# Performance work log

Hardware: AMD Instinct MI355X
Metric: run time of the kernel (lower is better)

Reference implementation:

```python
import jax, jax.numpy as jnp
import numpy as np

IN_CH, OUT_CH, K, N = 32, 64, 7, 64  # input_channels, output_channels, kernel_size, input_size


def _pad_kernel(kernel):
    # Replicates OpticalConv2dNew.process_inputs/__pad for K < N:
    # symmetric pad by (N-K)//2, then (0,1,0,1) if size still off by one.
    p = (N - K) // 2
    extra = 1 if (K + 2 * p) != N else 0
    return jnp.pad(kernel, ((0, 0), (0, 0), (p, p + extra), (p, p + extra)))


def _opt_conv(img, ker):
    # Ideal 4f optical convolution (FFT-based, circular): |fftshift(ifft2(fft2(ifftshift(x)) * fft2(ifftshift(h))))|
    ax = (-2, -1)
    F = jnp.fft.fft2(jnp.fft.ifftshift(img, axes=ax))      # (B,1,in,N,N) complex
    G = jnp.fft.fft2(jnp.fft.ifftshift(ker, axes=ax))      # (1,out,in,N,N) complex
    out = jnp.fft.fftshift(jnp.fft.ifft2(F * G), axes=ax)  # (B,out,in,N,N)
    return jnp.abs(out)


def setup_inputs() -> dict:
    key = jax.random.key(0)
    k1, k2 = jax.random.split(key)
    B = 8
    inputs = {
        "input": jax.random.normal(k1, (B, IN_CH, N, N), dtype=jnp.float32),
        # kaiming-uniform-like init for the learned kernel parameter
        "kernel": jax.random.uniform(k2, (OUT_CH, IN_CH, K, K), dtype=jnp.float32,
                                     minval=-1.0, maxval=1.0) * float(np.sqrt(6.0 / (IN_CH * K * K))),
    }
    return inputs


def reference(input, kernel):
    ker = _pad_kernel(kernel)                 # (out,in,N,N)
    img = input[:, None, :, :, :]             # (B,1,in,N,N) — broadcast instead of repeat/reshape
    ker = ker[None, :, :, :, :]               # (1,out,in,N,N)
    out = _opt_conv(img, ker)                 # (B,out,in,N,N) float32 (abs of complex)
    return jnp.sum(out, axis=2)               # sum over input channels -> (B,out,N,N)
```

## Files before the change

### kernel.cpp

```cpp
#include <hip/hip_runtime.h>

typedef __attribute__((ext_vector_type(8)))  short short8;
typedef __attribute__((ext_vector_type(16))) float f32x16;

namespace {

__device__ __forceinline__ unsigned short f2bf(float f) {
    unsigned int u = __float_as_uint(f);
    u += 0x7fffu + ((u >> 16) & 1u);
    return (unsigned short)(u >> 16);
}

__device__ __forceinline__ f32x16 zero16() {
    f32x16 z;
#pragma unroll
    for (int r = 0; r < 16; ++r) z[r] = 0.0f;
    return z;
}

__global__ void prep_B(const float* __restrict__ ker, uint4* __restrict__ B3) {
    int t    = blockIdx.x * 256 + threadIdx.x;
    int lane = t & 63;
    int kq   = (t >> 6) & 3;
    int ot   = (t >> 8) & 1;
    int ic   = t >> 9;
    int m = lane & 31, h = lane >> 5;
    int oc = ot * 32 + m;
    int a  = 2 * kq + h;
    unsigned int d[4] = {0u, 0u, 0u, 0u};
    if (a < 7) {
        const float* row = ker + ((oc * 32 + ic) * 49) + (6 - a) * 7;
        float v[8];
#pragma unroll
        for (int q = 0; q < 7; ++q) v[q] = row[6 - q];
        v[7] = 0.0f;
#pragma unroll
        for (int j = 0; j < 4; ++j)
            d[j] = (unsigned int)f2bf(v[2 * j]) | ((unsigned int)f2bf(v[2 * j + 1]) << 16);
    }
    B3[t] = make_uint4(d[0], d[1], d[2], d[3]);
}

__global__ __launch_bounds__(512, 4) void conv_mfma(
    const float* __restrict__ img,
    const uint4* __restrict__ B3,
    float* __restrict__ out)
{
    __shared__ unsigned int H[16128];

    const int bid  = blockIdx.x;
    const int y    = bid & 63;
    const int b    = bid >> 6;
    const int tid  = threadIdx.x;
    const int lane = tid & 63;
    const int w    = tid >> 6;
    const int xh   = w & 1;
    const int icg  = w >> 1;
    const int n31  = lane & 31;
    const int h    = lane >> 5;

    const float* base = img + (size_t)b * 32 * 4096;

    float v[28];
#pragma unroll
    for (int j = 0; j < 28; ++j) {
        const int pl  = 4 * w + j / 7;
        const int row = (y - 2 + (j % 7)) & 63;
        v[j] = base[pl * 4096 + row * 64 + lane];
    }
#pragma unroll
    for (int j = 0; j < 28; ++j) {
        const int pl = 4 * w + j / 7;
        const int r  = j % 7;
        const unsigned int hh = f2bf(v[j]);
        const unsigned int hn = (unsigned int)__shfl((int)hh, (lane + 1) & 63);
        const unsigned int dw = hh | (hn << 16);
        const int idx = pl * 504 + r * 72;
        H[idx + lane + 2] = dw;
        if (lane >= 62) H[idx + lane - 62] = dw;
        if (lane <= 5)  H[idx + lane + 66] = dw;
    }
    __syncthreads();

    f32x16 acc[2] = {zero16(), zero16()};
    const int xloc = 32 * xh + n31;
    const int hv   = h * 72;

#pragma unroll 2
    for (int ici = 0; ici < 8; ++ici) {
        const int ic = icg * 8 + ici;
        uint4 tf[8];
#pragma unroll
        for (int q = 0; q < 8; ++q)
            tf[q] = B3[ic * 512 + q * 64 + lane];

        short8 fr[4];
#pragma unroll
        for (int kq = 0; kq < 4; ++kq) {
            const int ad = ic * 504 + ((kq < 3) ? (2 * kq * 72 + hv) : 432) + xloc;
            uint4 t4 = make_uint4(H[ad], H[ad + 2], H[ad + 4], H[ad + 6]);
            fr[kq] = __builtin_bit_cast(short8, t4);
        }
#pragma unroll
        for (int ot = 0; ot < 2; ++ot) {
            f32x16 d = zero16();
#pragma unroll
            for (int kq = 0; kq < 4; ++kq)
                d = __builtin_amdgcn_mfma_f32_32x32x16_bf16(
                        __builtin_bit_cast(short8, tf[ot * 4 + kq]), fr[kq], d, 0, 0, 0);
#pragma unroll
            for (int r = 0; r < 16; ++r)
                acc[ot][r] += __builtin_fabsf(d[r]);
        }
    }

    float* P = (float*)H;
    __syncthreads();
    if (icg & 1) {
        const int rb = ((icg >> 1) * 2 + xh) * 2048;
#pragma unroll
        for (int ot = 0; ot < 2; ++ot)
#pragma unroll
            for (int rq = 0; rq < 4; ++rq)
                *(float4*)&P[rb + (ot * 4 + rq) * 256 + lane * 4] =
                    make_float4(acc[ot][rq * 4], acc[ot][rq * 4 + 1],
                                acc[ot][rq * 4 + 2], acc[ot][rq * 4 + 3]);
    }
    __syncthreads();
    if (!(icg & 1)) {
        const int rb = ((icg >> 1) * 2 + xh) * 2048;
#pragma unroll
        for (int ot = 0; ot < 2; ++ot)
#pragma unroll
            for (int rq = 0; rq < 4; ++rq)
#pragma unroll
                for (int i = 0; i < 4; ++i)
                    acc[ot][rq * 4 + i] += P[rb + (ot * 4 + rq) * 256 + lane * 4 + i];
    }
    if (icg == 2) {
        const int rb = (4 + xh) * 2048;
#pragma unroll
        for (int ot = 0; ot < 2; ++ot)
#pragma unroll
            for (int rq = 0; rq < 4; ++rq)
                *(float4*)&P[rb + (ot * 4 + rq) * 256 + lane * 4] =
                    make_float4(acc[ot][rq * 4], acc[ot][rq * 4 + 1],
                                acc[ot][rq * 4 + 2], acc[ot][rq * 4 + 3]);
    }
    __syncthreads();
    if (icg == 0) {
        const int rb = (4 + xh) * 2048;
#pragma unroll
        for (int ot = 0; ot < 2; ++ot)
#pragma unroll
            for (int reg = 0; reg < 16; ++reg) {
                const int oc = 32 * ot + (reg & 3) + 8 * (reg >> 2) + 4 * h;
                out[(size_t)(b * 64 + oc) * 4096 + y * 64 + xloc] =
                    acc[ot][reg] +
                    P[rb + (ot * 4 + (reg >> 2)) * 256 + lane * 4 + (reg & 3)];
            }
    }
}

}

extern "C" void kernel_launch(void* const* d_in, const int* in_sizes, int n_in,
                              void* d_out, int out_size, void* d_ws, size_t ws_size,
                              hipStream_t stream) {
    const float* img = (const float*)d_in[0];
    const float* ker = (const float*)d_in[1];
    float* out = (float*)d_out;
    uint4* B3 = (uint4*)d_ws;

    prep_B<<<dim3(64), dim3(256), 0, stream>>>(ker, B3);
    conv_mfma<<<dim3(512), dim3(512), 0, stream>>>(img, B3, out);
}
```

Measured before the change: 75.05 us.

## Split waves by output tile and input-channel half, prefetch kernel fragments

Each wave now owns one output-channel tile (ot) and half of the input channels (16), not both output tiles over a quarter of the input channels. This halves the per-wave accumulator and B-fragment registers and cuts the cross-wave reduction from two LDS passes to one. The loop is fully unrolled with a double-buffered register prefetch of the next channel's B fragments to hide global-load latency. Each wave still issues the same number of MFMAs, and the A fragments from LDS are now read twice per channel, once by each ot wave.

```diff
diff --git a/kernel.cpp b/kernel.cpp
--- a/kernel.cpp
+++ b/kernel.cpp
@@ -55,7 +55,8 @@
     const int lane = tid & 63;
     const int w    = tid >> 6;
     const int xh   = w & 1;
-    const int icg  = w >> 1;
+    const int ot   = (w >> 1) & 1;
+    const int ich  = w >> 2;
     const int n31  = lane & 31;
     const int h    = lane >> 5;
 
@@ -82,18 +83,25 @@
     }
     __syncthreads();
 
-    f32x16 acc[2] = {zero16(), zero16()};
+    f32x16 acc = zero16();
     const int xloc = 32 * xh + n31;
     const int hv   = h * 72;
+    const int ic0  = ich * 16;
+    const int qb   = ot * 4;
 
-#pragma unroll 2
-    for (int ici = 0; ici < 8; ++ici) {
-        const int ic = icg * 8 + ici;
-        uint4 tf[8];
+    uint4 tfC[4], tfN[4];
 #pragma unroll
-        for (int q = 0; q < 8; ++q)
-            tf[q] = B3[ic * 512 + q * 64 + lane];
+    for (int kq = 0; kq < 4; ++kq)
+        tfC[kq] = B3[ic0 * 512 + (qb + kq) * 64 + lane];
 
+#pragma unroll
+    for (int ici = 0; ici < 16; ++ici) {
+        const int ic = ic0 + ici;
+        if (ici < 15) {
+#pragma unroll
+            for (int kq = 0; kq < 4; ++kq)
+                tfN[kq] = B3[(ic + 1) * 512 + (qb + kq) * 64 + lane];
+        }
         short8 fr[4];
 #pragma unroll
         for (int kq = 0; kq < 4; ++kq) {
@@ -101,64 +109,35 @@
             uint4 t4 = make_uint4(H[ad], H[ad + 2], H[ad + 4], H[ad + 6]);
             fr[kq] = __builtin_bit_cast(short8, t4);
         }
+        f32x16 d = zero16();
 #pragma unroll
-        for (int ot = 0; ot < 2; ++ot) {
-            f32x16 d = zero16();
+        for (int kq = 0; kq < 4; ++kq)
+            d = __builtin_amdgcn_mfma_f32_32x32x16_bf16(
+                    __builtin_bit_cast(short8, tfC[kq]), fr[kq], d, 0, 0, 0);
 #pragma unroll
-            for (int kq = 0; kq < 4; ++kq)
-                d = __builtin_amdgcn_mfma_f32_32x32x16_bf16(
-                        __builtin_bit_cast(short8, tf[ot * 4 + kq]), fr[kq], d, 0, 0, 0);
+        for (int r = 0; r < 16; ++r)
+            acc[r] += __builtin_fabsf(d[r]);
 #pragma unroll
-            for (int r = 0; r < 16; ++r)
-                acc[ot][r] += __builtin_fabsf(d[r]);
-        }
+        for (int kq = 0; kq < 4; ++kq) tfC[kq] = tfN[kq];
     }
 
     float* P = (float*)H;
     __syncthreads();
-    if (icg & 1) {
-        const int rb = ((icg >> 1) * 2 + xh) * 2048;
+    if (ich == 1) {
+        const int rb = (xh * 2 + ot) * 1024;
 #pragma unroll
-        for (int ot = 0; ot < 2; ++ot)
-#pragma unroll
-            for (int rq = 0; rq < 4; ++rq)
-                *(float4*)&P[rb + (ot * 4 + rq) * 256 + lane * 4] =
-                    make_float4(acc[ot][rq * 4], acc[ot][rq * 4 + 1],
-                                acc[ot][rq * 4 + 2], acc[ot][rq * 4 + 3]);
+        for (int r = 0; r < 16; ++r)
+            P[rb + r * 64 + lane] = acc[r];
     }
     __syncthreads();
-    if (!(icg & 1)) {
-        const int rb = ((icg >> 1) * 2 + xh) * 2048;
+    if (ich == 0) {
+        const int rb = (xh * 2 + ot) * 1024;
 #pragma unroll
-        for (int ot = 0; ot < 2; ++ot)
-#pragma unroll
-            for (int rq = 0; rq < 4; ++rq)
-#pragma unroll
-                for (int i = 0; i < 4; ++i)
-                    acc[ot][rq * 4 + i] += P[rb + (ot * 4 + rq) * 256 + lane * 4 + i];
-    }
-    if (icg == 2) {
-        const int rb = (4 + xh) * 2048;
-#pragma unroll
-        for (int ot = 0; ot < 2; ++ot)
-#pragma unroll
-            for (int rq = 0; rq < 4; ++rq)
-                *(float4*)&P[rb + (ot * 4 + rq) * 256 + lane * 4] =
-                    make_float4(acc[ot][rq * 4], acc[ot][rq * 4 + 1],
-                                acc[ot][rq * 4 + 2], acc[ot][rq * 4 + 3]);
-    }
-    __syncthreads();
-    if (icg == 0) {
-        const int rb = (4 + xh) * 2048;
-#pragma unroll
-        for (int ot = 0; ot < 2; ++ot)
-#pragma unroll
-            for (int reg = 0; reg < 16; ++reg) {
-                const int oc = 32 * ot + (reg & 3) + 8 * (reg >> 2) + 4 * h;
-                out[(size_t)(b * 64 + oc) * 4096 + y * 64 + xloc] =
-                    acc[ot][reg] +
-                    P[rb + (ot * 4 + (reg >> 2)) * 256 + lane * 4 + (reg & 3)];
-            }
+        for (int reg = 0; reg < 16; ++reg) {
+            const int oc = 32 * ot + (reg & 3) + 8 * (reg >> 2) + 4 * h;
+            out[(size_t)(b * 64 + oc) * 4096 + y * 64 + xloc] =
+                acc[reg] + P[rb + reg * 64 + lane];
+        }
     }
 }
 
```

New measurement: 74.21 us. No clear change (-1.1%).
